# Kernel tuning notes

Hardware: AMD Instinct MI355X
Metric: run time of the kernel (lower is better)

Reference implementation:

```python
import jax, jax.numpy as jnp
import numpy as np

EPS = 1e-6

def _resize_mask_nearest(mask, h, w):
    # mask: (B, H, W) float in {0,1} -> (B, 1, h, w), F.interpolate mode='nearest' semantics
    B, H, W = mask.shape
    ih = (jnp.arange(h) * H) // h  # floor(dst * H/h)
    iw = (jnp.arange(w) * W) // w
    m = mask[:, ih][:, :, iw]
    return m[:, None]  # (B,1,h,w)

def masked_avg_pool(feat, mask_rs):
    # feat: (B,C,H,W), mask_rs: (B,1,H,W) -> (B,C)
    num = (feat * mask_rs).sum(axis=(2, 3))
    den = mask_rs.sum(axis=(2, 3)) + EPS
    return num / den

def compute_P(proto_fg, proto_bg, R):
    # proto_*: (B,d); R: (2,d) learnable anchors -> P: (B,d,d)
    B, d = proto_fg.shape
    C = jnp.stack([proto_bg, proto_fg], axis=1)                     # (B,2,d)
    C = C / (jnp.sqrt((C ** 2).sum(axis=2, keepdims=True)) + EPS)
    Rn = R / (jnp.sqrt((R ** 2).sum(axis=1, keepdims=True)) + EPS)  # (2,d)
    Rb = jnp.broadcast_to(Rn[None], (B, 2, d))
    P = jnp.matmul(jnp.linalg.pinv(C), Rb)                          # (B,d,d)
    return jnp.swapaxes(P, 1, 2)

def apply_P_to_feat(P, feat):
    b, d, h, w = feat.shape
    out = jnp.einsum('bij,bjn->bin', P, feat.reshape(b, d, h * w))
    return out.reshape(b, d, h, w)

def masked_topk_tokens(feat, mask_rs, k):
    # feat: (B,C,H,W), mask_rs: (B,1,H,W) -> tokens (B,k,C); deterministic L2-norm top-k
    b, c, h, w = feat.shape
    scores = jnp.sqrt((feat ** 2).sum(axis=1)).reshape(b, -1)       # (B,HW)
    mask_flat = mask_rs.reshape(b, -1)
    valid = mask_flat.sum(axis=1) > 0
    mask_flat = jnp.where(valid[:, None], mask_flat, 1.0)           # fallback_to_full
    scores = jnp.where(mask_flat >= 0.5, scores, -jnp.inf)
    _, idx = jax.lax.top_k(scores, k)                               # (B,k)
    tok = jnp.take_along_axis(feat.reshape(b, c, -1), idx[:, None, :], axis=2)  # (B,C,k)
    return jnp.swapaxes(tok, 1, 2)                                  # (B,k,C)

def setup_inputs() -> dict:
    key = jax.random.key(0)
    ks = jax.random.split(key, 12)
    B, d = 8, 256
    sizes = [(64, 64), (32, 32), (16, 16)]
    inp = {}
    for i, (h, w) in enumerate(sizes):
        inp[f'q{i+1}'] = jax.random.normal(ks[i], (B, d, h, w), jnp.float32)
        inp[f's{i+1}'] = jax.random.normal(ks[3 + i], (B, d, h, w), jnp.float32)
        # kaiming_normal fan_in=d, linear -> std = 1/sqrt(d)
        inp[f'r{i+1}'] = jax.random.normal(ks[6 + i], (2, d), jnp.float32) / jnp.sqrt(jnp.float32(d))
    inp['support_mask'] = jax.random.randint(ks[9], (B, 512, 512), 0, 2, jnp.int32)
    inp['k'] = 32
    return inp

def reference(q1, q2, q3, s1, s2, s3, r1, r2, r3, support_mask, k):
    mask = support_mask.astype(jnp.float32)  # (B,H,W)
    qs = [q1, q2, q3]
    ss = [s1, s2, s3]
    rs = [r1, r2, r3]
    parts_q, parts_s, pfgs, pbgs = [], [], [], []
    mask_rs0 = None
    s_t0 = None
    for li in range(3):
        q, s, R = qs[li], ss[li], rs[li]
        b, d, h, w = s.shape
        mask_rs = _resize_mask_nearest(mask, h, w)
        proto_fg = masked_avg_pool(s, mask_rs)
        proto_bg = masked_avg_pool(s, 1.0 - mask_rs)
        P = compute_P(proto_fg, proto_bg, R)
        q_t = apply_P_to_feat(P, q)
        s_t = apply_P_to_feat(P, s)
        parts_q.append(q_t.reshape(b, d, -1))
        parts_s.append(s_t.reshape(b, d, -1))
        pfgs.append(masked_avg_pool(s_t, mask_rs))
        pbgs.append(masked_avg_pool(s_t, 1.0 - mask_rs))
        if li == 0:
            mask_rs0, s_t0 = mask_rs, s_t
    tokens = masked_topk_tokens(s_t0, mask_rs0, k)  # (B,k,d)
    # pack everything into one (B, d, N) array: q_t flats, s_t flats, fg/bg protos, tokens
    packed = jnp.concatenate(
        parts_q + parts_s
        + [jnp.stack(pfgs, axis=2), jnp.stack(pbgs, axis=2), jnp.swapaxes(tokens, 1, 2)],
        axis=2)
    return packed
```

## Files before the change

### kernel.cpp

```cpp
#include <hip/hip_runtime.h>
#include <math.h>

#define NTOT 10790
#define NTOT2 5395
#define EPSF 1e-6f

__device__ __forceinline__ float block_reduce_sum(float v, float* red) {
    int tid = threadIdx.x;
    red[tid] = v; __syncthreads();
    for (int off = 128; off > 0; off >>= 1) {
        if (tid < off) red[tid] += red[tid + off];
        __syncthreads();
    }
    float r = red[0];
    __syncthreads();
    return r;
}

__device__ __forceinline__ bool kvGreater(float as, int ai, float bs, int bi) {
    return (as > bs) || (as == bs && ai < bi);
}

__device__ __forceinline__ void sort64(float& s, int& i, int lane) {
    #pragma unroll
    for (int k = 2; k <= 64; k <<= 1) {
        #pragma unroll
        for (int j = k >> 1; j > 0; j >>= 1) {
            float os = __shfl_xor(s, j, 64);
            int   oi = __shfl_xor(i, j, 64);
            bool lower = (lane & j) == 0;
            bool blockDesc = (lane & k) == 0;
            bool keepG = (blockDesc == lower);
            bool og = kvGreater(os, oi, s, i);
            if (og == keepG) { s = os; i = oi; }
        }
    }
}

__device__ __forceinline__ void merge64(float& as, int& ai, float bs, int bi, int lane) {
    float rbs = __shfl(bs, 63 - lane, 64);
    int   rbi = __shfl(bi, 63 - lane, 64);
    if (!kvGreater(as, ai, rbs, rbi)) { as = rbs; ai = rbi; }
    #pragma unroll
    for (int j = 32; j > 0; j >>= 1) {
        float os = __shfl_xor(as, j, 64);
        int   oi = __shfl_xor(ai, j, 64);
        bool lower = (lane & j) == 0;
        bool og = kvGreater(os, oi, as, ai);
        if (og == lower) { as = os; ai = oi; }
    }
}

__global__ __launch_bounds__(256) void mask_kernel(const int* __restrict__ mask,
                                                   float* __restrict__ wsm0,
                                                   float* __restrict__ wsm1,
                                                   float* __restrict__ wsm2,
                                                   float* __restrict__ msum) {
    int level = blockIdx.x, b = blockIdx.y, tid = threadIdx.x;
    int h = 64 >> level, w = h, S = 8 << level, HW = h * w;
    float* wsm = (level == 0) ? wsm0 : ((level == 1) ? wsm1 : wsm2);
    const int* mb = mask + (size_t)b * 512 * 512;
    float acc = 0.f;
    for (int n = tid; n < HW; n += 256) {
        int y = n / w, x = n - y * w;
        float mv = (float)mb[y * S * 512 + x * S];
        wsm[b * HW + n] = mv;
        acc += mv;
    }
    __shared__ float red[256];
    float s = block_reduce_sum(acc, red);
    if (tid == 0) msum[b * 3 + level] = s;
}

__global__ __launch_bounds__(256) void sreduce_kernel(const float* __restrict__ s0,
                                                      const float* __restrict__ s1,
                                                      const float* __restrict__ s2,
                                                      const float* __restrict__ wsm0,
                                                      const float* __restrict__ wsm1,
                                                      const float* __restrict__ wsm2,
                                                      float* __restrict__ fgnum,
                                                      float* __restrict__ tot) {
    int c = blockIdx.x, b = blockIdx.y, level = blockIdx.z, tid = threadIdx.x;
    int HW = 4096 >> (2 * level);
    int HW4 = HW >> 2;
    const float* s = (level == 0) ? s0 : ((level == 1) ? s1 : s2);
    const float* wsm = (level == 0) ? wsm0 : ((level == 1) ? wsm1 : wsm2);
    const float4* sb4 = (const float4*)(s + ((size_t)(b * 256) + c) * HW);
    const float4* mb4 = (const float4*)(wsm + (size_t)b * HW);
    float af = 0.f, at = 0.f;
    for (int i = tid; i < HW4; i += 256) {
        float4 x = sb4[i];
        float4 m = mb4[i];
        at += (x.x + x.y) + (x.z + x.w);
        af = fmaf(x.x, m.x, fmaf(x.y, m.y, fmaf(x.z, m.z, fmaf(x.w, m.w, af))));
    }
    __shared__ float redA[256], redB[256];
    redA[tid] = af; redB[tid] = at; __syncthreads();
    for (int off = 128; off > 0; off >>= 1) {
        if (tid < off) { redA[tid] += redA[tid + off]; redB[tid] += redB[tid + off]; }
        __syncthreads();
    }
    if (tid == 0) {
        int base = (level * 8 + b) * 256 + c;
        fgnum[base] = redA[0];
        tot[base]   = redB[0];
    }
}

__global__ __launch_bounds__(256) void protos_kernel(const float* __restrict__ R0p,
                                                     const float* __restrict__ R1p,
                                                     const float* __restrict__ R2p,
                                                     const float* __restrict__ fgnum,
                                                     const float* __restrict__ tot,
                                                     const float* __restrict__ msum,
                                                     float* __restrict__ c0v,
                                                     float* __restrict__ c1v,
                                                     float* __restrict__ rn0v,
                                                     float* __restrict__ rn1v,
                                                     float* __restrict__ minv,
                                                     float* __restrict__ rg) {
    int b = blockIdx.x, level = blockIdx.y, c = threadIdx.x;
    int HW = 4096 >> (2 * level);
    const float* R = (level == 0) ? R0p : ((level == 1) ? R1p : R2p);
    __shared__ float red[256];
    int base = (level * 8 + b) * 256;
    float ms = msum[b * 3 + level];
    float denf = ms + EPSF;
    float denb = ((float)HW - ms) + EPSF;
    float fg = fgnum[base + c];
    float tt = tot[base + c];
    float pf = fg / denf;
    float pb = (tt - fg) / denb;
    float nf = block_reduce_sum(pf * pf, red);
    float nb = block_reduce_sum(pb * pb, red);
    float C1 = pf / (sqrtf(nf) + EPSF);
    float C0 = pb / (sqrtf(nb) + EPSF);
    c0v[base + c] = C0;
    c1v[base + c] = C1;
    float r0 = R[c], r1 = R[256 + c];
    float n0 = block_reduce_sum(r0 * r0, red);
    float n1 = block_reduce_sum(r1 * r1, red);
    float rr = block_reduce_sum(r0 * r1, red);
    float i0 = 1.0f / (sqrtf(n0) + EPSF);
    float i1 = 1.0f / (sqrtf(n1) + EPSF);
    rn0v[base + c] = r0 * i0;
    rn1v[base + c] = r1 * i1;
    float a  = block_reduce_sum(C0 * C0, red);
    float bb = block_reduce_sum(C0 * C1, red);
    float cc = block_reduce_sum(C1 * C1, red);
    if (c == 0) {
        float det = a * cc - bb * bb;
        float id = 1.0f / det;
        float* M = minv + (level * 8 + b) * 4;
        M[0] = cc * id; M[1] = -bb * id; M[2] = -bb * id; M[3] = a * id;
        float* G = rg + (level * 8 + b) * 4;
        G[0] = n0 * i0 * i0;
        G[1] = rr * i0 * i1;
        G[2] = n1 * i1 * i1;
    }
}

__global__ __launch_bounds__(256) void transform_kernel(const float* __restrict__ q0,
                                                        const float* __restrict__ q1,
                                                        const float* __restrict__ q2,
                                                        const float* __restrict__ s0,
                                                        const float* __restrict__ s1,
                                                        const float* __restrict__ s2,
                                                        float* __restrict__ out,
                                                        const float* __restrict__ c0v,
                                                        const float* __restrict__ c1v,
                                                        const float* __restrict__ rn0v,
                                                        const float* __restrict__ rn1v,
                                                        const float* __restrict__ minv,
                                                        const float* __restrict__ wsm0,
                                                        const float* __restrict__ wsm1,
                                                        const float* __restrict__ wsm2,
                                                        float* __restrict__ vbuf,
                                                        float* __restrict__ partials) {
    int b = blockIdx.y;
    int xb = blockIdx.x;
    int is_s = (xb >= 42);
    if (is_s) xb -= 42;
    int level, blk;
    if (xb < 32)      { level = 0; blk = xb; }
    else if (xb < 40) { level = 1; blk = xb - 32; }
    else              { level = 2; blk = xb - 40; }
    int HW = 4096 >> (2 * level);
    int HW4 = HW >> 2;
    const float* x = is_s ? ((level == 0) ? s0 : ((level == 1) ? s1 : s2))
                          : ((level == 0) ? q0 : ((level == 1) ? q1 : q2));
    const float* wsm = (level == 0) ? wsm0 : ((level == 1) ? wsm1 : wsm2);
    const int qoffs[3] = {0, 4096, 5120};
    const int soffs[3] = {5376, 9472, 10496};
    int col_off = is_s ? soffs[level] : qoffs[level];
    int n0 = blk * 128;
    int tid = threadIdx.x;

    __shared__ float sc0[256], sc1[256], srn0[256], srn1[256];
    __shared__ float st0[8][32][4], st1[8][32][4];
    __shared__ float4 su4[64];
    __shared__ float pred[2][4];
    int base = (level * 8 + b) * 256;
    sc0[tid] = c0v[base + tid];
    sc1[tid] = c1v[base + tid];
    srn0[tid] = rn0v[base + tid];
    srn1[tid] = rn1v[base + tid];
    __syncthreads();

    const float4* xb4 = (const float4*)(x + (size_t)(b * 256) * HW);
    int cg = tid >> 5, l = tid & 31;
    size_t idx0 = (size_t)(cg * 32) * HW4 + (n0 >> 2) + l;
    float t0x = 0, t0y = 0, t0z = 0, t0w = 0;
    float t1x = 0, t1y = 0, t1z = 0, t1w = 0;
    #pragma unroll 8
    for (int i = 0; i < 32; i++) {
        int c = cg * 32 + i;
        float4 xv = xb4[idx0 + (size_t)i * HW4];
        float a = sc0[c], bq = sc1[c];
        t0x = fmaf(a, xv.x, t0x); t0y = fmaf(a, xv.y, t0y);
        t0z = fmaf(a, xv.z, t0z); t0w = fmaf(a, xv.w, t0w);
        t1x = fmaf(bq, xv.x, t1x); t1y = fmaf(bq, xv.y, t1y);
        t1z = fmaf(bq, xv.z, t1z); t1w = fmaf(bq, xv.w, t1w);
    }
    st0[cg][l][0] = t0x; st0[cg][l][1] = t0y; st0[cg][l][2] = t0z; st0[cg][l][3] = t0w;
    st1[cg][l][0] = t1x; st1[cg][l][1] = t1y; st1[cg][l][2] = t1z; st1[cg][l][3] = t1w;
    __syncthreads();

    if (tid < 128) {
        int p = tid;
        const float* f0 = &st0[0][p >> 2][p & 3];
        const float* f1 = &st1[0][p >> 2][p & 3];
        float a0 = 0.f, a1 = 0.f;
        #pragma unroll
        for (int g2 = 0; g2 < 8; g2++) {
            a0 += f0[g2 * 128];
            a1 += f1[g2 * 128];
        }
        const float* M = minv + (level * 8 + b) * 4;
        float u0 = M[0] * a0 + M[1] * a1;
        float u1 = M[1] * a0 + M[3] * a1;
        ((float2*)su4)[p] = make_float2(u0, u1);
        if (is_s) {
            int n = n0 + p;
            if (level == 0) {
                *(float2*)&vbuf[((size_t)b * 4096 + n) * 2] = make_float2(u0, u1);
            }
            float m = wsm[b * HW + n];
            float s0r = m * u0, s1r = m * u1, s2r = u0, s3r = u1;
            for (int off = 32; off > 0; off >>= 1) {
                s0r += __shfl_down(s0r, off, 64);
                s1r += __shfl_down(s1r, off, 64);
                s2r += __shfl_down(s2r, off, 64);
                s3r += __shfl_down(s3r, off, 64);
            }
            if ((tid & 63) == 0) {
                int wv = tid >> 6;
                pred[wv][0] = s0r; pred[wv][1] = s1r;
                pred[wv][2] = s2r; pred[wv][3] = s3r;
            }
        }
    }
    __syncthreads();
    if (is_s && tid == 0) {
        float* pp = partials + (((level * 8 + b) * 64) + blk) * 4;
        pp[0] = pred[0][0] + pred[1][0];
        pp[1] = pred[0][1] + pred[1][1];
        pp[2] = pred[0][2] + pred[1][2];
        pp[3] = pred[0][3] + pred[1][3];
    }

    int g = tid >> 6, slot = tid & 63;
    float4 sq = su4[slot];
    float2* ob2 = (float2*)out + ((size_t)(b * 256) + g * 64) * NTOT2
                  + ((col_off + n0) >> 1) + slot;
    #pragma unroll 8
    for (int i = 0; i < 64; i++) {
        int c = g * 64 + i;
        float r0 = srn0[c], r1 = srn1[c];
        ob2[(size_t)i * NTOT2] = make_float2(fmaf(r0, sq.x, r1 * sq.y),
                                             fmaf(r0, sq.z, r1 * sq.w));
    }
}

__global__ __launch_bounds__(1024) void final_kernel(float* __restrict__ out,
                                                     const float* __restrict__ v,
                                                     const float* __restrict__ wsm0,
                                                     const float* __restrict__ msum,
                                                     const float* __restrict__ rn0v,
                                                     const float* __restrict__ rn1v,
                                                     const float* __restrict__ rg,
                                                     const float* __restrict__ partials) {
    int b = blockIdx.x, tid = threadIdx.x;
    int w = tid >> 6, lane = tid & 63;
    __shared__ float lds_s[16 * 64];
    __shared__ int   lds_i[16 * 64];
    __shared__ float2 suv[32];
    __shared__ float sA[3][4];

    float A = rg[b * 4 + 0], B = rg[b * 4 + 1], C = rg[b * 4 + 2];
    bool validmask = msum[b * 3 + 0] > 0.0f;

    float as; int ai;
    #pragma unroll
    for (int c4 = 0; c4 < 4; ++c4) {
        int n = (w * 4 + c4) * 64 + lane;
        float2 uv = *(const float2*)&v[((size_t)b * 4096 + n) * 2];
        float ss = fmaxf(A * uv.x * uv.x + 2.0f * B * uv.x * uv.y + C * uv.y * uv.y, 0.0f);
        float s = sqrtf(ss);
        float m = validmask ? wsm0[b * 4096 + n] : 1.0f;
        s = (m >= 0.5f) ? s : -INFINITY;
        int i = n;
        sort64(s, i, lane);
        if (c4 == 0) { as = s; ai = i; }
        else merge64(as, ai, s, i, lane);
    }
    lds_s[w * 64 + lane] = as;
    lds_i[w * 64 + lane] = ai;
    __syncthreads();

    for (int act = 8; act >= 1; act >>= 1) {
        float ms_; int mi_;
        bool active = (w < act);
        if (active) {
            ms_ = lds_s[(2 * w) * 64 + lane];
            mi_ = lds_i[(2 * w) * 64 + lane];
            float bs_ = lds_s[(2 * w + 1) * 64 + lane];
            int   bi_ = lds_i[(2 * w + 1) * 64 + lane];
            merge64(ms_, mi_, bs_, bi_, lane);
        }
        __syncthreads();
        if (active) {
            lds_s[w * 64 + lane] = ms_;
            lds_i[w * 64 + lane] = mi_;
        }
        __syncthreads();
    }

    if (tid < 32) {
        int idx = lds_i[tid];
        suv[tid] = *(const float2*)&v[((size_t)b * 4096 + idx) * 2];
    }
    __syncthreads();

    int c = tid >> 2, qd = tid & 3;
    float r0 = rn0v[b * 256 + c], r1 = rn1v[b * 256 + c];
    float2* o2 = (float2*)out + ((size_t)(b * 256) + c) * NTOT2 + 5379 + qd * 4;
    #pragma unroll
    for (int t = 0; t < 4; ++t) {
        float2 uv0 = suv[qd * 8 + 2 * t];
        float2 uv1 = suv[qd * 8 + 2 * t + 1];
        o2[t] = make_float2(fmaf(r0, uv0.x, r1 * uv0.y),
                            fmaf(r0, uv1.x, r1 * uv1.y));
    }

    if (tid < 3) {
        int lv = tid;
        const int HWl[3] = {4096, 1024, 256};
        const int nbl[3] = {32, 8, 2};
        const float* pp = partials + ((size_t)(lv * 8 + b) * 64) * 4;
        float t0 = 0, t1 = 0, t2 = 0, t3 = 0;
        for (int i = 0; i < nbl[lv]; i++) {
            t0 += pp[i * 4 + 0]; t1 += pp[i * 4 + 1];
            t2 += pp[i * 4 + 2]; t3 += pp[i * 4 + 3];
        }
        float ms = msum[b * 3 + lv];
        float denf = ms + EPSF;
        float denb = ((float)HWl[lv] - ms) + EPSF;
        sA[lv][0] = t0 / denf;
        sA[lv][1] = t1 / denf;
        sA[lv][2] = (t2 - t0) / denb;
        sA[lv][3] = (t3 - t1) / denb;
    }
    __syncthreads();
    if (tid < 768) {
        int lv = tid >> 8, cc = tid & 255;
        int base = (lv * 8 + b) * 256;
        float rr0 = rn0v[base + cc], rr1 = rn1v[base + cc];
        size_t row = ((size_t)(b * 256) + cc) * NTOT;
        out[row + 10752 + lv] = fmaf(rr0, sA[lv][0], rr1 * sA[lv][1]);
        out[row + 10755 + lv] = fmaf(rr0, sA[lv][2], rr1 * sA[lv][3]);
    }
}

extern "C" void kernel_launch(void* const* d_in, const int* in_sizes, int n_in,
                              void* d_out, int out_size, void* d_ws, size_t ws_size,
                              hipStream_t stream) {
    const float* q0 = (const float*)d_in[0];
    const float* s0 = (const float*)d_in[1];
    const float* r0 = (const float*)d_in[2];
    const float* q1 = (const float*)d_in[3];
    const float* s1 = (const float*)d_in[4];
    const float* r1 = (const float*)d_in[5];
    const float* q2 = (const float*)d_in[6];
    const float* s2 = (const float*)d_in[7];
    const float* r2 = (const float*)d_in[8];
    const int* mask = (const int*)d_in[9];
    float* out = (float*)d_out;
    float* W = (float*)d_ws;

    float* wsm0 = W;
    float* wsm1 = W + 32768;
    float* wsm2 = W + 40960;
    float* msum = W + 43008;
    float* fgnum = W + 43040;
    float* tot  = W + 49184;
    float* c0v  = W + 55328;
    float* c1v  = W + 61472;
    float* rn0v = W + 67616;
    float* rn1v = W + 73760;
    float* minv = W + 79904;
    float* rg   = W + 80000;
    float* vbuf = W + 80128;
    float* part = W + 145664;

    mask_kernel<<<dim3(3, 8), 256, 0, stream>>>(mask, wsm0, wsm1, wsm2, msum);

    sreduce_kernel<<<dim3(256, 8, 3), 256, 0, stream>>>(s0, s1, s2, wsm0, wsm1, wsm2,
                                                        fgnum, tot);

    protos_kernel<<<dim3(8, 3), 256, 0, stream>>>(r0, r1, r2, fgnum, tot, msum,
                                                  c0v, c1v, rn0v, rn1v, minv, rg);

    transform_kernel<<<dim3(84, 8), 256, 0, stream>>>(q0, q1, q2, s0, s1, s2, out,
                                                      c0v, c1v, rn0v, rn1v, minv,
                                                      wsm0, wsm1, wsm2, vbuf, part);

    final_kernel<<<8, 1024, 0, stream>>>(out, vbuf, wsm0, msum, rn0v, rn1v, rg, part);
}
```

Measured before the change: 77.36 us.

## Drop mask kernel by sampling mask inline; shrink transform blocks to one wave

Removes the separate mask-downsampling kernel and its workspace buffers. Consumers now read the strided nearest-neighbour samples straight from the full-resolution int mask, and sreduce's c==0 blocks compute the mask sums. The transform kernel is restructured from 256-thread blocks with a cross-group LDS reduction to 64-thread blocks, where each lane walks all 256 channels for two pixels. This removes shared-memory staging and barriers but leaves only 672 single-wave blocks and long serial per-lane loops, which risks underusing the GPU and exposing latency. Strided gathers from the large mask replace contiguous reads of the small buffer.

```diff
diff --git a/kernel.cpp b/kernel.cpp
--- a/kernel.cpp
+++ b/kernel.cpp
@@ -51,48 +51,29 @@
     }
 }
 
-__global__ __launch_bounds__(256) void mask_kernel(const int* __restrict__ mask,
-                                                   float* __restrict__ wsm0,
-                                                   float* __restrict__ wsm1,
-                                                   float* __restrict__ wsm2,
-                                                   float* __restrict__ msum) {
-    int level = blockIdx.x, b = blockIdx.y, tid = threadIdx.x;
-    int h = 64 >> level, w = h, S = 8 << level, HW = h * w;
-    float* wsm = (level == 0) ? wsm0 : ((level == 1) ? wsm1 : wsm2);
-    const int* mb = mask + (size_t)b * 512 * 512;
-    float acc = 0.f;
-    for (int n = tid; n < HW; n += 256) {
-        int y = n / w, x = n - y * w;
-        float mv = (float)mb[y * S * 512 + x * S];
-        wsm[b * HW + n] = mv;
-        acc += mv;
-    }
-    __shared__ float red[256];
-    float s = block_reduce_sum(acc, red);
-    if (tid == 0) msum[b * 3 + level] = s;
-}
-
 __global__ __launch_bounds__(256) void sreduce_kernel(const float* __restrict__ s0,
                                                       const float* __restrict__ s1,
                                                       const float* __restrict__ s2,
-                                                      const float* __restrict__ wsm0,
-                                                      const float* __restrict__ wsm1,
-                                                      const float* __restrict__ wsm2,
+                                                      const int* __restrict__ mask,
+                                                      float* __restrict__ msum,
                                                       float* __restrict__ fgnum,
                                                       float* __restrict__ tot) {
     int c = blockIdx.x, b = blockIdx.y, level = blockIdx.z, tid = threadIdx.x;
-    int HW = 4096 >> (2 * level);
-    int HW4 = HW >> 2;
+    int w = 64 >> level, HW = w * w, HW4 = HW >> 2, S = 8 << level;
     const float* s = (level == 0) ? s0 : ((level == 1) ? s1 : s2);
-    const float* wsm = (level == 0) ? wsm0 : ((level == 1) ? wsm1 : wsm2);
+    const int* mb = mask + (size_t)b * 512 * 512;
     const float4* sb4 = (const float4*)(s + ((size_t)(b * 256) + c) * HW);
-    const float4* mb4 = (const float4*)(wsm + (size_t)b * HW);
-    float af = 0.f, at = 0.f;
+    bool writer = (c == 0);
+    float af = 0.f, at = 0.f, am = 0.f;
     for (int i = tid; i < HW4; i += 256) {
+        int n = 4 * i; int y = n / w; int x0 = n - y * w;
+        const int* mrow = mb + (size_t)y * S * 512 + (size_t)x0 * S;
+        float m0 = (float)mrow[0], m1 = (float)mrow[S];
+        float m2 = (float)mrow[2 * S], m3 = (float)mrow[3 * S];
         float4 x = sb4[i];
-        float4 m = mb4[i];
         at += (x.x + x.y) + (x.z + x.w);
-        af = fmaf(x.x, m.x, fmaf(x.y, m.y, fmaf(x.z, m.z, fmaf(x.w, m.w, af))));
+        af = fmaf(x.x, m0, fmaf(x.y, m1, fmaf(x.z, m2, fmaf(x.w, m3, af))));
+        if (writer) am += (m0 + m1) + (m2 + m3);
     }
     __shared__ float redA[256], redB[256];
     redA[tid] = af; redB[tid] = at; __syncthreads();
@@ -100,10 +81,12 @@
         if (tid < off) { redA[tid] += redA[tid + off]; redB[tid] += redB[tid + off]; }
         __syncthreads();
     }
-    if (tid == 0) {
-        int base = (level * 8 + b) * 256 + c;
-        fgnum[base] = redA[0];
-        tot[base]   = redB[0];
+    int base = (level * 8 + b) * 256;
+    if (tid == 0) { fgnum[base + c] = redA[0]; tot[base + c] = redB[0]; }
+    __syncthreads();
+    if (writer) {
+        float amsum = block_reduce_sum(am, redA);
+        if (tid == 0) msum[b * 3 + level] = amsum;
     }
 }
 
@@ -160,131 +143,101 @@
     }
 }
 
-__global__ __launch_bounds__(256) void transform_kernel(const float* __restrict__ q0,
-                                                        const float* __restrict__ q1,
-                                                        const float* __restrict__ q2,
-                                                        const float* __restrict__ s0,
-                                                        const float* __restrict__ s1,
-                                                        const float* __restrict__ s2,
-                                                        float* __restrict__ out,
-                                                        const float* __restrict__ c0v,
-                                                        const float* __restrict__ c1v,
-                                                        const float* __restrict__ rn0v,
-                                                        const float* __restrict__ rn1v,
-                                                        const float* __restrict__ minv,
-                                                        const float* __restrict__ wsm0,
-                                                        const float* __restrict__ wsm1,
-                                                        const float* __restrict__ wsm2,
-                                                        float* __restrict__ vbuf,
-                                                        float* __restrict__ partials) {
-    int b = blockIdx.y;
-    int xb = blockIdx.x;
-    int is_s = (xb >= 42);
-    if (is_s) xb -= 42;
-    int level, blk;
-    if (xb < 32)      { level = 0; blk = xb; }
-    else if (xb < 40) { level = 1; blk = xb - 32; }
-    else              { level = 2; blk = xb - 40; }
+__global__ __launch_bounds__(64) void transform_kernel(const float* __restrict__ q0,
+                                                       const float* __restrict__ q1,
+                                                       const float* __restrict__ q2,
+                                                       const float* __restrict__ s0,
+                                                       const float* __restrict__ s1,
+                                                       const float* __restrict__ s2,
+                                                       const int* __restrict__ mask,
+                                                       float* __restrict__ out,
+                                                       const float* __restrict__ c0v,
+                                                       const float* __restrict__ c1v,
+                                                       const float* __restrict__ rn0v,
+                                                       const float* __restrict__ rn1v,
+                                                       const float* __restrict__ minv,
+                                                       float* __restrict__ vbuf,
+                                                       float* __restrict__ partials) {
+    int b = blockIdx.y, t = blockIdx.x, lane = threadIdx.x;
+    int is_s, blk, level;
+    if (t < 32)      { level = 0; is_s = 0; blk = t; }
+    else if (t < 64) { level = 0; is_s = 1; blk = t - 32; }
+    else if (t < 72) { level = 1; is_s = 0; blk = t - 64; }
+    else if (t < 80) { level = 1; is_s = 1; blk = t - 72; }
+    else if (t < 82) { level = 2; is_s = 0; blk = t - 80; }
+    else             { level = 2; is_s = 1; blk = t - 82; }
     int HW = 4096 >> (2 * level);
-    int HW4 = HW >> 2;
+    int HW2 = HW >> 1;
     const float* x = is_s ? ((level == 0) ? s0 : ((level == 1) ? s1 : s2))
                           : ((level == 0) ? q0 : ((level == 1) ? q1 : q2));
-    const float* wsm = (level == 0) ? wsm0 : ((level == 1) ? wsm1 : wsm2);
     const int qoffs[3] = {0, 4096, 5120};
     const int soffs[3] = {5376, 9472, 10496};
     int col_off = is_s ? soffs[level] : qoffs[level];
     int n0 = blk * 128;
-    int tid = threadIdx.x;
+    int base = (level * 8 + b) * 256;
 
     __shared__ float sc0[256], sc1[256], srn0[256], srn1[256];
-    __shared__ float st0[8][32][4], st1[8][32][4];
-    __shared__ float4 su4[64];
-    __shared__ float pred[2][4];
-    int base = (level * 8 + b) * 256;
-    sc0[tid] = c0v[base + tid];
-    sc1[tid] = c1v[base + tid];
-    srn0[tid] = rn0v[base + tid];
-    srn1[tid] = rn1v[base + tid];
-    __syncthreads();
-
-    const float4* xb4 = (const float4*)(x + (size_t)(b * 256) * HW);
-    int cg = tid >> 5, l = tid & 31;
-    size_t idx0 = (size_t)(cg * 32) * HW4 + (n0 >> 2) + l;
-    float t0x = 0, t0y = 0, t0z = 0, t0w = 0;
-    float t1x = 0, t1y = 0, t1z = 0, t1w = 0;
+    #pragma unroll
+    for (int i = lane; i < 256; i += 64) {
+        sc0[i] = c0v[base + i];
+        sc1[i] = c1v[base + i];
+        srn0[i] = rn0v[base + i];
+        srn1[i] = rn1v[base + i];
+    }
+    __syncthreads();
+
+    const float2* x2 = (const float2*)(x + (size_t)(b * 256) * HW) + (n0 >> 1) + lane;
+    float a0x = 0.f, a0y = 0.f, a1x = 0.f, a1y = 0.f;
+    #pragma unroll 16
+    for (int c = 0; c < 256; c++) {
+        float2 xv = x2[(size_t)c * HW2];
+        float ca = sc0[c], cb = sc1[c];
+        a0x = fmaf(ca, xv.x, a0x); a0y = fmaf(ca, xv.y, a0y);
+        a1x = fmaf(cb, xv.x, a1x); a1y = fmaf(cb, xv.y, a1y);
+    }
+    const float* M = minv + (level * 8 + b) * 4;
+    float M0 = M[0], M1 = M[1], M3 = M[3];
+    float u0x = M0 * a0x + M1 * a1x, u1x = M1 * a0x + M3 * a1x;
+    float u0y = M0 * a0y + M1 * a1y, u1y = M1 * a0y + M3 * a1y;
+
+    int n = n0 + 2 * lane;
+    if (is_s) {
+        if (level == 0) {
+            *(float4*)&vbuf[((size_t)b * 4096 + n) * 2] = make_float4(u0x, u1x, u0y, u1y);
+        }
+        int wdim = 64 >> level, S = 8 << level, ysh = 6 - level;
+        const int* mb = mask + (size_t)b * 512 * 512;
+        float m0 = (float)mb[(size_t)(n >> ysh) * S * 512 + (size_t)(n & (wdim - 1)) * S];
+        int n2 = n + 1;
+        float m1 = (float)mb[(size_t)(n2 >> ysh) * S * 512 + (size_t)(n2 & (wdim - 1)) * S];
+        float p0 = m0 * u0x + m1 * u0y;
+        float p1 = m0 * u1x + m1 * u1y;
+        float p2 = u0x + u0y;
+        float p3 = u1x + u1y;
+        for (int off = 32; off > 0; off >>= 1) {
+            p0 += __shfl_down(p0, off, 64);
+            p1 += __shfl_down(p1, off, 64);
+            p2 += __shfl_down(p2, off, 64);
+            p3 += __shfl_down(p3, off, 64);
+        }
+        if (lane == 0) {
+            float* pp = partials + (((level * 8 + b) * 64) + blk) * 4;
+            pp[0] = p0; pp[1] = p1; pp[2] = p2; pp[3] = p3;
+        }
+    }
+
+    float2* ob2 = (float2*)out + (size_t)(b * 256) * NTOT2 + ((col_off + n0) >> 1) + lane;
     #pragma unroll 8
-    for (int i = 0; i < 32; i++) {
-        int c = cg * 32 + i;
-        float4 xv = xb4[idx0 + (size_t)i * HW4];
-        float a = sc0[c], bq = sc1[c];
-        t0x = fmaf(a, xv.x, t0x); t0y = fmaf(a, xv.y, t0y);
-        t0z = fmaf(a, xv.z, t0z); t0w = fmaf(a, xv.w, t0w);
-        t1x = fmaf(bq, xv.x, t1x); t1y = fmaf(bq, xv.y, t1y);
-        t1z = fmaf(bq, xv.z, t1z); t1w = fmaf(bq, xv.w, t1w);
-    }
-    st0[cg][l][0] = t0x; st0[cg][l][1] = t0y; st0[cg][l][2] = t0z; st0[cg][l][3] = t0w;
-    st1[cg][l][0] = t1x; st1[cg][l][1] = t1y; st1[cg][l][2] = t1z; st1[cg][l][3] = t1w;
-    __syncthreads();
-
-    if (tid < 128) {
-        int p = tid;
-        const float* f0 = &st0[0][p >> 2][p & 3];
-        const float* f1 = &st1[0][p >> 2][p & 3];
-        float a0 = 0.f, a1 = 0.f;
-        #pragma unroll
-        for (int g2 = 0; g2 < 8; g2++) {
-            a0 += f0[g2 * 128];
-            a1 += f1[g2 * 128];
-        }
-        const float* M = minv + (level * 8 + b) * 4;
-        float u0 = M[0] * a0 + M[1] * a1;
-        float u1 = M[1] * a0 + M[3] * a1;
-        ((float2*)su4)[p] = make_float2(u0, u1);
-        if (is_s) {
-            int n = n0 + p;
-            if (level == 0) {
-                *(float2*)&vbuf[((size_t)b * 4096 + n) * 2] = make_float2(u0, u1);
-            }
-            float m = wsm[b * HW + n];
-            float s0r = m * u0, s1r = m * u1, s2r = u0, s3r = u1;
-            for (int off = 32; off > 0; off >>= 1) {
-                s0r += __shfl_down(s0r, off, 64);
-                s1r += __shfl_down(s1r, off, 64);
-                s2r += __shfl_down(s2r, off, 64);
-                s3r += __shfl_down(s3r, off, 64);
-            }
-            if ((tid & 63) == 0) {
-                int wv = tid >> 6;
-                pred[wv][0] = s0r; pred[wv][1] = s1r;
-                pred[wv][2] = s2r; pred[wv][3] = s3r;
-            }
-        }
-    }
-    __syncthreads();
-    if (is_s && tid == 0) {
-        float* pp = partials + (((level * 8 + b) * 64) + blk) * 4;
-        pp[0] = pred[0][0] + pred[1][0];
-        pp[1] = pred[0][1] + pred[1][1];
-        pp[2] = pred[0][2] + pred[1][2];
-        pp[3] = pred[0][3] + pred[1][3];
-    }
-
-    int g = tid >> 6, slot = tid & 63;
-    float4 sq = su4[slot];
-    float2* ob2 = (float2*)out + ((size_t)(b * 256) + g * 64) * NTOT2
-                  + ((col_off + n0) >> 1) + slot;
-    #pragma unroll 8
-    for (int i = 0; i < 64; i++) {
-        int c = g * 64 + i;
+    for (int c = 0; c < 256; c++) {
         float r0 = srn0[c], r1 = srn1[c];
-        ob2[(size_t)i * NTOT2] = make_float2(fmaf(r0, sq.x, r1 * sq.y),
-                                             fmaf(r0, sq.z, r1 * sq.w));
+        ob2[(size_t)c * NTOT2] = make_float2(fmaf(r0, u0x, r1 * u1x),
+                                             fmaf(r0, u0y, r1 * u1y));
     }
 }
 
 __global__ __launch_bounds__(1024) void final_kernel(float* __restrict__ out,
                                                      const float* __restrict__ v,
-                                                     const float* __restrict__ wsm0,
+                                                     const int* __restrict__ mask,
                                                      const float* __restrict__ msum,
                                                      const float* __restrict__ rn0v,
                                                      const float* __restrict__ rn1v,
@@ -299,6 +252,7 @@
 
     float A = rg[b * 4 + 0], B = rg[b * 4 + 1], C = rg[b * 4 + 2];
     bool validmask = msum[b * 3 + 0] > 0.0f;
+    const int* mb = mask + (size_t)b * 512 * 512;
 
     float as; int ai;
     #pragma unroll
@@ -307,7 +261,7 @@
         float2 uv = *(const float2*)&v[((size_t)b * 4096 + n) * 2];
         float ss = fmaxf(A * uv.x * uv.x + 2.0f * B * uv.x * uv.y + C * uv.y * uv.y, 0.0f);
         float s = sqrtf(ss);
-        float m = validmask ? wsm0[b * 4096 + n] : 1.0f;
+        float m = validmask ? (float)mb[((n >> 6) << 12) + ((n & 63) << 3)] : 1.0f;
         s = (m >= 0.5f) ? s : -INFINITY;
         int i = n;
         sort64(s, i, lane);
@@ -398,32 +352,27 @@
     float* out = (float*)d_out;
     float* W = (float*)d_ws;
 
-    float* wsm0 = W;
-    float* wsm1 = W + 32768;
-    float* wsm2 = W + 40960;
-    float* msum = W + 43008;
-    float* fgnum = W + 43040;
-    float* tot  = W + 49184;
-    float* c0v  = W + 55328;
-    float* c1v  = W + 61472;
-    float* rn0v = W + 67616;
-    float* rn1v = W + 73760;
-    float* minv = W + 79904;
-    float* rg   = W + 80000;
-    float* vbuf = W + 80128;
-    float* part = W + 145664;
-
-    mask_kernel<<<dim3(3, 8), 256, 0, stream>>>(mask, wsm0, wsm1, wsm2, msum);
-
-    sreduce_kernel<<<dim3(256, 8, 3), 256, 0, stream>>>(s0, s1, s2, wsm0, wsm1, wsm2,
-                                                        fgnum, tot);
+    float* msum = W;
+    float* fgnum = W + 32;
+    float* tot  = W + 6176;
+    float* c0v  = W + 12320;
+    float* c1v  = W + 18464;
+    float* rn0v = W + 24608;
+    float* rn1v = W + 30752;
+    float* minv = W + 36896;
+    float* rg   = W + 36992;
+    float* vbuf = W + 37120;
+    float* part = W + 102656;
+
+    sreduce_kernel<<<dim3(256, 8, 3), 256, 0, stream>>>(s0, s1, s2, mask,
+                                                        msum, fgnum, tot);
 
     protos_kernel<<<dim3(8, 3), 256, 0, stream>>>(r0, r1, r2, fgnum, tot, msum,
                                                   c0v, c1v, rn0v, rn1v, minv, rg);
 
-    transform_kernel<<<dim3(84, 8), 256, 0, stream>>>(q0, q1, q2, s0, s1, s2, out,
-                                                      c0v, c1v, rn0v, rn1v, minv,
-                                                      wsm0, wsm1, wsm2, vbuf, part);
-
-    final_kernel<<<8, 1024, 0, stream>>>(out, vbuf, wsm0, msum, rn0v, rn1v, rg, part);
-}
+    transform_kernel<<<dim3(84, 8), 64, 0, stream>>>(q0, q1, q2, s0, s1, s2, mask, out,
+                                                     c0v, c1v, rn0v, rn1v, minv,
+                                                     vbuf, part);
+
+    final_kernel<<<8, 1024, 0, stream>>>(out, vbuf, mask, msum, rn0v, rn1v, rg, part);
+}
```

Measured after the change: 96.58 us. 24.8% more time.

## Halve transform kernel pixel tile to double grid size

Applied to the files above, without the earlier changes.

Each transform block now handles 64 pixels instead of 128, doubling the grid from 84x8 to 168x8 blocks. The thread mapping changes to 16 pixel-quads by 16 channel groups, and the per-block partial sums are written directly from the single reducing wave. The aim is more blocks in flight across the many CUs of the GPU, to improve memory-level parallelism for a bandwidth-bound pass. In exchange each block does more redundant coefficient loads and writes shorter output row segments per channel (256 bytes instead of 512), which may lower write efficiency.

```diff
diff --git a/kernel.cpp b/kernel.cpp
--- a/kernel.cpp
+++ b/kernel.cpp
@@ -179,12 +179,12 @@
                                                         float* __restrict__ partials) {
     int b = blockIdx.y;
     int xb = blockIdx.x;
-    int is_s = (xb >= 42);
-    if (is_s) xb -= 42;
+    int is_s = (xb >= 84);
+    if (is_s) xb -= 84;
     int level, blk;
-    if (xb < 32)      { level = 0; blk = xb; }
-    else if (xb < 40) { level = 1; blk = xb - 32; }
-    else              { level = 2; blk = xb - 40; }
+    if (xb < 64)      { level = 0; blk = xb; }
+    else if (xb < 80) { level = 1; blk = xb - 64; }
+    else              { level = 2; blk = xb - 80; }
     int HW = 4096 >> (2 * level);
     int HW4 = HW >> 2;
     const float* x = is_s ? ((level == 0) ? s0 : ((level == 1) ? s1 : s2))
@@ -193,13 +193,12 @@
     const int qoffs[3] = {0, 4096, 5120};
     const int soffs[3] = {5376, 9472, 10496};
     int col_off = is_s ? soffs[level] : qoffs[level];
-    int n0 = blk * 128;
+    int n0 = blk * 64;
     int tid = threadIdx.x;
 
     __shared__ float sc0[256], sc1[256], srn0[256], srn1[256];
-    __shared__ float st0[8][32][4], st1[8][32][4];
-    __shared__ float4 su4[64];
-    __shared__ float pred[2][4];
+    __shared__ float st0[16][64], st1[16][64];
+    __shared__ float2 su[64];
     int base = (level * 8 + b) * 256;
     sc0[tid] = c0v[base + tid];
     sc1[tid] = c1v[base + tid];
@@ -208,13 +207,13 @@
     __syncthreads();
 
     const float4* xb4 = (const float4*)(x + (size_t)(b * 256) * HW);
-    int cg = tid >> 5, l = tid & 31;
-    size_t idx0 = (size_t)(cg * 32) * HW4 + (n0 >> 2) + l;
+    int px4 = tid & 15, cg = tid >> 4;
+    size_t idx0 = (size_t)(cg * 16) * HW4 + (n0 >> 2) + px4;
     float t0x = 0, t0y = 0, t0z = 0, t0w = 0;
     float t1x = 0, t1y = 0, t1z = 0, t1w = 0;
-    #pragma unroll 8
-    for (int i = 0; i < 32; i++) {
-        int c = cg * 32 + i;
+    #pragma unroll
+    for (int i = 0; i < 16; i++) {
+        int c = cg * 16 + i;
         float4 xv = xb4[idx0 + (size_t)i * HW4];
         float a = sc0[c], bq = sc1[c];
         t0x = fmaf(a, xv.x, t0x); t0y = fmaf(a, xv.y, t0y);
@@ -222,63 +221,55 @@
         t1x = fmaf(bq, xv.x, t1x); t1y = fmaf(bq, xv.y, t1y);
         t1z = fmaf(bq, xv.z, t1z); t1w = fmaf(bq, xv.w, t1w);
     }
-    st0[cg][l][0] = t0x; st0[cg][l][1] = t0y; st0[cg][l][2] = t0z; st0[cg][l][3] = t0w;
-    st1[cg][l][0] = t1x; st1[cg][l][1] = t1y; st1[cg][l][2] = t1z; st1[cg][l][3] = t1w;
-    __syncthreads();
-
-    if (tid < 128) {
+    st0[cg][px4 * 4 + 0] = t0x; st0[cg][px4 * 4 + 1] = t0y;
+    st0[cg][px4 * 4 + 2] = t0z; st0[cg][px4 * 4 + 3] = t0w;
+    st1[cg][px4 * 4 + 0] = t1x; st1[cg][px4 * 4 + 1] = t1y;
+    st1[cg][px4 * 4 + 2] = t1z; st1[cg][px4 * 4 + 3] = t1w;
+    __syncthreads();
+
+    if (tid < 64) {
         int p = tid;
-        const float* f0 = &st0[0][p >> 2][p & 3];
-        const float* f1 = &st1[0][p >> 2][p & 3];
         float a0 = 0.f, a1 = 0.f;
         #pragma unroll
-        for (int g2 = 0; g2 < 8; g2++) {
-            a0 += f0[g2 * 128];
-            a1 += f1[g2 * 128];
+        for (int g2 = 0; g2 < 16; g2++) {
+            a0 += st0[g2][p];
+            a1 += st1[g2][p];
         }
         const float* M = minv + (level * 8 + b) * 4;
         float u0 = M[0] * a0 + M[1] * a1;
         float u1 = M[1] * a0 + M[3] * a1;
-        ((float2*)su4)[p] = make_float2(u0, u1);
+        su[p] = make_float2(u0, u1);
         if (is_s) {
             int n = n0 + p;
             if (level == 0) {
                 *(float2*)&vbuf[((size_t)b * 4096 + n) * 2] = make_float2(u0, u1);
             }
             float m = wsm[b * HW + n];
-            float s0r = m * u0, s1r = m * u1, s2r = u0, s3r = u1;
+            float p0 = m * u0, p1 = m * u1, p2 = u0, p3 = u1;
             for (int off = 32; off > 0; off >>= 1) {
-                s0r += __shfl_down(s0r, off, 64);
-                s1r += __shfl_down(s1r, off, 64);
-                s2r += __shfl_down(s2r, off, 64);
-                s3r += __shfl_down(s3r, off, 64);
+                p0 += __shfl_down(p0, off, 64);
+                p1 += __shfl_down(p1, off, 64);
+                p2 += __shfl_down(p2, off, 64);
+                p3 += __shfl_down(p3, off, 64);
             }
-            if ((tid & 63) == 0) {
-                int wv = tid >> 6;
-                pred[wv][0] = s0r; pred[wv][1] = s1r;
-                pred[wv][2] = s2r; pred[wv][3] = s3r;
+            if (p == 0) {
+                float* pp = partials + (((level * 8 + b) * 64) + blk) * 4;
+                pp[0] = p0; pp[1] = p1; pp[2] = p2; pp[3] = p3;
             }
         }
     }
     __syncthreads();
-    if (is_s && tid == 0) {
-        float* pp = partials + (((level * 8 + b) * 64) + blk) * 4;
-        pp[0] = pred[0][0] + pred[1][0];
-        pp[1] = pred[0][1] + pred[1][1];
-        pp[2] = pred[0][2] + pred[1][2];
-        pp[3] = pred[0][3] + pred[1][3];
-    }
-
-    int g = tid >> 6, slot = tid & 63;
-    float4 sq = su4[slot];
-    float2* ob2 = (float2*)out + ((size_t)(b * 256) + g * 64) * NTOT2
+
+    int slot = tid & 31, cgw = tid >> 5;
+    float2 sqa = su[2 * slot], sqb = su[2 * slot + 1];
+    float2* ob2 = (float2*)out + ((size_t)(b * 256) + cgw * 32) * NTOT2
                   + ((col_off + n0) >> 1) + slot;
     #pragma unroll 8
-    for (int i = 0; i < 64; i++) {
-        int c = g * 64 + i;
+    for (int i = 0; i < 32; i++) {
+        int c = cgw * 32 + i;
         float r0 = srn0[c], r1 = srn1[c];
-        ob2[(size_t)i * NTOT2] = make_float2(fmaf(r0, sq.x, r1 * sq.y),
-                                             fmaf(r0, sq.z, r1 * sq.w));
+        ob2[(size_t)i * NTOT2] = make_float2(fmaf(r0, sqa.x, r1 * sqa.y),
+                                             fmaf(r0, sqb.x, r1 * sqb.y));
     }
 }
 
@@ -356,7 +347,7 @@
     if (tid < 3) {
         int lv = tid;
         const int HWl[3] = {4096, 1024, 256};
-        const int nbl[3] = {32, 8, 2};
+        const int nbl[3] = {64, 16, 4};
         const float* pp = partials + ((size_t)(lv * 8 + b) * 64) * 4;
         float t0 = 0, t1 = 0, t2 = 0, t3 = 0;
         for (int i = 0; i < nbl[lv]; i++) {
@@ -421,9 +412,9 @@
     protos_kernel<<<dim3(8, 3), 256, 0, stream>>>(r0, r1, r2, fgnum, tot, msum,
                                                   c0v, c1v, rn0v, rn1v, minv, rg);
 
-    transform_kernel<<<dim3(84, 8), 256, 0, stream>>>(q0, q1, q2, s0, s1, s2, out,
-                                                      c0v, c1v, rn0v, rn1v, minv,
-                                                      wsm0, wsm1, wsm2, vbuf, part);
+    transform_kernel<<<dim3(168, 8), 256, 0, stream>>>(q0, q1, q2, s0, s1, s2, out,
+                                                       c0v, c1v, rn0v, rn1v, minv,
+                                                       wsm0, wsm1, wsm2, vbuf, part);
 
     final_kernel<<<8, 1024, 0, stream>>>(out, vbuf, wsm0, msum, rn0v, rn1v, rg, part);
 }
```

Measured after the change: 85.11 us. 10.0% more time.

## Split transform kernel into separate dot-product and reconstruction kernels

Applied to the files above, without the earlier changes.

The fused transform kernel is split in two. The first kernel computes the per-pixel 2-D coefficients (u0, u1) and the mask partial sums, and writes all coefficients to a workspace buffer. A second kernel reads them back and writes the rank-2 reconstruction to the output. The final kernel now reads level-0 support coefficients from the same buffer. This likely aims to keep each kernel's read or write phase separate for better occupancy, at the cost of an extra launch and a small intermediate buffer round-trip.

```diff
diff --git a/kernel.cpp b/kernel.cpp
--- a/kernel.cpp
+++ b/kernel.cpp
@@ -160,23 +160,20 @@
     }
 }
 
-__global__ __launch_bounds__(256) void transform_kernel(const float* __restrict__ q0,
-                                                        const float* __restrict__ q1,
-                                                        const float* __restrict__ q2,
-                                                        const float* __restrict__ s0,
-                                                        const float* __restrict__ s1,
-                                                        const float* __restrict__ s2,
-                                                        float* __restrict__ out,
-                                                        const float* __restrict__ c0v,
-                                                        const float* __restrict__ c1v,
-                                                        const float* __restrict__ rn0v,
-                                                        const float* __restrict__ rn1v,
-                                                        const float* __restrict__ minv,
-                                                        const float* __restrict__ wsm0,
-                                                        const float* __restrict__ wsm1,
-                                                        const float* __restrict__ wsm2,
-                                                        float* __restrict__ vbuf,
-                                                        float* __restrict__ partials) {
+__global__ __launch_bounds__(256) void dots_kernel(const float* __restrict__ q0,
+                                                   const float* __restrict__ q1,
+                                                   const float* __restrict__ q2,
+                                                   const float* __restrict__ s0,
+                                                   const float* __restrict__ s1,
+                                                   const float* __restrict__ s2,
+                                                   const float* __restrict__ c0v,
+                                                   const float* __restrict__ c1v,
+                                                   const float* __restrict__ minv,
+                                                   const float* __restrict__ wsm0,
+                                                   const float* __restrict__ wsm1,
+                                                   const float* __restrict__ wsm2,
+                                                   float* __restrict__ ubuf,
+                                                   float* __restrict__ partials) {
     int b = blockIdx.y;
     int xb = blockIdx.x;
     int is_s = (xb >= 42);
@@ -196,15 +193,12 @@
     int n0 = blk * 128;
     int tid = threadIdx.x;
 
-    __shared__ float sc0[256], sc1[256], srn0[256], srn1[256];
+    __shared__ float sc0[256], sc1[256];
     __shared__ float st0[8][32][4], st1[8][32][4];
-    __shared__ float4 su4[64];
     __shared__ float pred[2][4];
     int base = (level * 8 + b) * 256;
     sc0[tid] = c0v[base + tid];
     sc1[tid] = c1v[base + tid];
-    srn0[tid] = rn0v[base + tid];
-    srn1[tid] = rn1v[base + tid];
     __syncthreads();
 
     const float4* xb4 = (const float4*)(x + (size_t)(b * 256) * HW);
@@ -239,24 +233,21 @@
         const float* M = minv + (level * 8 + b) * 4;
         float u0 = M[0] * a0 + M[1] * a1;
         float u1 = M[1] * a0 + M[3] * a1;
-        ((float2*)su4)[p] = make_float2(u0, u1);
+        ((float2*)ubuf)[(size_t)b * 10752 + col_off + n0 + p] = make_float2(u0, u1);
         if (is_s) {
             int n = n0 + p;
-            if (level == 0) {
-                *(float2*)&vbuf[((size_t)b * 4096 + n) * 2] = make_float2(u0, u1);
-            }
             float m = wsm[b * HW + n];
-            float s0r = m * u0, s1r = m * u1, s2r = u0, s3r = u1;
+            float p0 = m * u0, p1 = m * u1, p2 = u0, p3 = u1;
             for (int off = 32; off > 0; off >>= 1) {
-                s0r += __shfl_down(s0r, off, 64);
-                s1r += __shfl_down(s1r, off, 64);
-                s2r += __shfl_down(s2r, off, 64);
-                s3r += __shfl_down(s3r, off, 64);
+                p0 += __shfl_down(p0, off, 64);
+                p1 += __shfl_down(p1, off, 64);
+                p2 += __shfl_down(p2, off, 64);
+                p3 += __shfl_down(p3, off, 64);
             }
             if ((tid & 63) == 0) {
                 int wv = tid >> 6;
-                pred[wv][0] = s0r; pred[wv][1] = s1r;
-                pred[wv][2] = s2r; pred[wv][3] = s3r;
+                pred[wv][0] = p0; pred[wv][1] = p1;
+                pred[wv][2] = p2; pred[wv][3] = p3;
             }
         }
     }
@@ -268,22 +259,45 @@
         pp[2] = pred[0][2] + pred[1][2];
         pp[3] = pred[0][3] + pred[1][3];
     }
-
-    int g = tid >> 6, slot = tid & 63;
-    float4 sq = su4[slot];
-    float2* ob2 = (float2*)out + ((size_t)(b * 256) + g * 64) * NTOT2
-                  + ((col_off + n0) >> 1) + slot;
+}
+
+__global__ __launch_bounds__(256) void recon_kernel(float* __restrict__ out,
+                                                    const float* __restrict__ rn0v,
+                                                    const float* __restrict__ rn1v,
+                                                    const float* __restrict__ ubuf) {
+    int b = blockIdx.y;
+    int xb = blockIdx.x;
+    int is_s = (xb >= 42);
+    if (is_s) xb -= 42;
+    int level, blk;
+    if (xb < 32)      { level = 0; blk = xb; }
+    else if (xb < 40) { level = 1; blk = xb - 32; }
+    else              { level = 2; blk = xb - 40; }
+    const int qoffs[3] = {0, 4096, 5120};
+    const int soffs[3] = {5376, 9472, 10496};
+    int col = (is_s ? soffs[level] : qoffs[level]) + blk * 128;
+    int tid = threadIdx.x;
+    int base = (level * 8 + b) * 256;
+
+    __shared__ float srn0[256], srn1[256];
+    srn0[tid] = rn0v[base + tid];
+    srn1[tid] = rn1v[base + tid];
+    __syncthreads();
+
+    int slot = tid & 63, g = tid >> 6;
+    float4 uq = ((const float4*)ubuf)[(((size_t)b * 10752 + col) >> 1) + slot];
+    float2* ob2 = (float2*)out + ((size_t)(b * 256) + g * 64) * NTOT2 + (col >> 1) + slot;
     #pragma unroll 8
     for (int i = 0; i < 64; i++) {
         int c = g * 64 + i;
         float r0 = srn0[c], r1 = srn1[c];
-        ob2[(size_t)i * NTOT2] = make_float2(fmaf(r0, sq.x, r1 * sq.y),
-                                             fmaf(r0, sq.z, r1 * sq.w));
+        ob2[(size_t)i * NTOT2] = make_float2(fmaf(r0, uq.x, r1 * uq.y),
+                                             fmaf(r0, uq.z, r1 * uq.w));
     }
 }
 
 __global__ __launch_bounds__(1024) void final_kernel(float* __restrict__ out,
-                                                     const float* __restrict__ v,
+                                                     const float* __restrict__ ubuf,
                                                      const float* __restrict__ wsm0,
                                                      const float* __restrict__ msum,
                                                      const float* __restrict__ rn0v,
@@ -297,6 +311,7 @@
     __shared__ float2 suv[32];
     __shared__ float sA[3][4];
 
+    const float2* ub = (const float2*)ubuf + (size_t)b * 10752 + 5376;
     float A = rg[b * 4 + 0], B = rg[b * 4 + 1], C = rg[b * 4 + 2];
     bool validmask = msum[b * 3 + 0] > 0.0f;
 
@@ -304,7 +319,7 @@
     #pragma unroll
     for (int c4 = 0; c4 < 4; ++c4) {
         int n = (w * 4 + c4) * 64 + lane;
-        float2 uv = *(const float2*)&v[((size_t)b * 4096 + n) * 2];
+        float2 uv = ub[n];
         float ss = fmaxf(A * uv.x * uv.x + 2.0f * B * uv.x * uv.y + C * uv.y * uv.y, 0.0f);
         float s = sqrtf(ss);
         float m = validmask ? wsm0[b * 4096 + n] : 1.0f;
@@ -337,8 +352,7 @@
     }
 
     if (tid < 32) {
-        int idx = lds_i[tid];
-        suv[tid] = *(const float2*)&v[((size_t)b * 4096 + idx) * 2];
+        suv[tid] = ub[lds_i[tid]];
     }
     __syncthreads();
 
@@ -410,8 +424,8 @@
     float* rn1v = W + 73760;
     float* minv = W + 79904;
     float* rg   = W + 80000;
-    float* vbuf = W + 80128;
-    float* part = W + 145664;
+    float* ubuf = W + 80128;
+    float* part = W + 252160;
 
     mask_kernel<<<dim3(3, 8), 256, 0, stream>>>(mask, wsm0, wsm1, wsm2, msum);
 
@@ -421,9 +435,11 @@
     protos_kernel<<<dim3(8, 3), 256, 0, stream>>>(r0, r1, r2, fgnum, tot, msum,
                                                   c0v, c1v, rn0v, rn1v, minv, rg);
 
-    transform_kernel<<<dim3(84, 8), 256, 0, stream>>>(q0, q1, q2, s0, s1, s2, out,
-                                                      c0v, c1v, rn0v, rn1v, minv,
-                                                      wsm0, wsm1, wsm2, vbuf, part);
-
-    final_kernel<<<8, 1024, 0, stream>>>(out, vbuf, wsm0, msum, rn0v, rn1v, rg, part);
-}
+    dots_kernel<<<dim3(84, 8), 256, 0, stream>>>(q0, q1, q2, s0, s1, s2,
+                                                 c0v, c1v, minv,
+                                                 wsm0, wsm1, wsm2, ubuf, part);
+
+    recon_kernel<<<dim3(84, 8), 256, 0, stream>>>(out, rn0v, rn1v, ubuf);
+
+    final_kernel<<<8, 1024, 0, stream>>>(out, ubuf, wsm0, msum, rn0v, rn1v, rg, part);
+}
```

Result: slower. 81.60 us (+5.5%).
